# Kernel tuning notes

Measured on AMD Instinct MI355X. Metric: run time of the kernel, lower is better.

The kernel has to match this reference:

```python
import jax, jax.numpy as jnp
import numpy as np

B, S, HID = 1, 2048, 4096
H, HKV = 32, 8
D = HID // H          # 128
G = H // HKV          # 4 query heads per kv head (GQA)


def setup_inputs() -> dict:
    key = jax.random.key(0)
    ks = jax.random.split(key, 5)
    hidden_states = jax.random.normal(ks[0], (B, S, HID), dtype=jnp.float32)
    # additive causal mask: 0 on/below diagonal, large negative above
    causal = jnp.tril(jnp.ones((S, S), dtype=bool))
    attention_mask = jnp.where(causal, 0.0, -1e9).astype(jnp.float32)[None, None]
    sc = 0.02
    wq = jax.random.normal(ks[1], (HID, H * D), dtype=jnp.float32) * sc
    wk = jax.random.normal(ks[2], (HID, HKV * D), dtype=jnp.float32) * sc
    wv = jax.random.normal(ks[3], (HID, HKV * D), dtype=jnp.float32) * sc
    wo = jax.random.normal(ks[4], (H * D, HID), dtype=jnp.float32) * sc
    return {"hidden_states": hidden_states, "attention_mask": attention_mask,
            "wq": wq, "wk": wk, "wv": wv, "wo": wo}


def reference(hidden_states, attention_mask, wq, wk, wv, wo):
    # projections (lora_rank=0 path: plain dense, no bias)
    q = hidden_states @ wq                      # [B,S,H*D]
    k = hidden_states @ wk                      # [B,S,HKV*D]
    v = hidden_states @ wv                      # [B,S,HKV*D]
    # split heads; group query heads by their kv head: head h -> (h//G, h%G)
    q = q.reshape(B, S, HKV, G, D).transpose(0, 2, 3, 1, 4)   # [B,HKV,G,S,D]
    k = k.reshape(B, S, HKV, D).transpose(0, 2, 1, 3)          # [B,HKV,S,D]
    v = v.reshape(B, S, HKV, D).transpose(0, 2, 1, 3)          # [B,HKV,S,D]
    scale = 1.0 / jnp.sqrt(jnp.float32(D))
    # explicit S x S scores (as in source), with GQA kv broadcast over G
    scores = jnp.einsum('bkgsd,bktd->bkgst', q, k) * scale     # [B,HKV,G,S,S]
    scores = scores + attention_mask[:, :, None]               # broadcast over G
    probs = jax.nn.softmax(scores, axis=-1)
    attn = jnp.einsum('bkgst,bktd->bkgsd', probs, v)           # [B,HKV,G,S,D]
    attn = attn.transpose(0, 3, 1, 2, 4).reshape(B, S, H * D)  # [B,S,H*D]
    return attn @ wo                                           # [B,S,HID]
```

## Files before the change

kernel.cpp:

```cpp
#include <hip/hip_runtime.h>
#include <hip/hip_bf16.h>

#define S_LEN 2048
#define HID 4096
#define NH 32
#define NKV 8
#define HD 128
#define LDQKV 6144

typedef __bf16 bf16x8 __attribute__((ext_vector_type(8)));
typedef __bf16 bf16x4 __attribute__((ext_vector_type(4)));
typedef float f32x4 __attribute__((ext_vector_type(4)));

#define GLD16(gp, lp)                                                                   \
    __builtin_amdgcn_global_load_lds((const __attribute__((address_space(1))) void*)(gp), \
                                     (__attribute__((address_space(3))) void*)(lp), 16, 0, 0)

__global__ void cast_bf16_kernel(const float* __restrict__ x, __bf16* __restrict__ y, int n) {
    int i = (blockIdx.x * blockDim.x + threadIdx.x) * 4;
    if (i < n) {
        float4 v = *reinterpret_cast<const float4*>(x + i);
        bf16x4 o;
        o.x = (__bf16)v.x; o.y = (__bf16)v.y; o.z = (__bf16)v.z; o.w = (__bf16)v.w;
        *reinterpret_cast<bf16x4*>(y + i) = o;
    }
}

__global__ void transpose_cast_kernel(const float* __restrict__ W, __bf16* __restrict__ WT,
                                      int K, int N, float scale) {
    __shared__ float tile[32][33];
    int bx = blockIdx.x;
    int by = blockIdx.y;
    int tx = threadIdx.x;
    int ty = threadIdx.y;
    int n = bx * 32 + tx;
#pragma unroll
    for (int i = 0; i < 4; i++) {
        int k = by * 32 + ty + i * 8;
        tile[ty + i * 8][tx] = W[(size_t)k * N + n];
    }
    __syncthreads();
    int k2 = by * 32 + tx;
#pragma unroll
    for (int i = 0; i < 4; i++) {
        int n2 = bx * 32 + ty + i * 8;
        WT[(size_t)n2 * K + k2] = (__bf16)(tile[tx][ty + i * 8] * scale);
    }
}

__global__ void transpose_bf16_kernel(const __bf16* __restrict__ V, int ldin,
                                      __bf16* __restrict__ VT, int ldout) {
    __shared__ __bf16 tile[32][33];
    int bx = blockIdx.x;
    int by = blockIdx.y;
    int tx = threadIdx.x;
    int ty = threadIdx.y;
#pragma unroll
    for (int i = 0; i < 4; i++)
        tile[ty + i * 8][tx] = V[(size_t)(by * 32 + ty + i * 8) * ldin + bx * 32 + tx];
    __syncthreads();
#pragma unroll
    for (int i = 0; i < 4; i++)
        VT[(size_t)(bx * 32 + ty + i * 8) * ldout + by * 32 + tx] = tile[tx][ty + i * 8];
}

template <typename OUT_T>
__global__ __launch_bounds__(256) void gemm_bt_kernel(const __bf16* __restrict__ A, int lda,
                                                      const __bf16* __restrict__ BT, int ldb,
                                                      OUT_T* __restrict__ C, int ldc, int K) {
    __shared__ __bf16 As[128 * 32];
    __shared__ __bf16 Bs[128 * 32];
    int n0 = blockIdx.x * 128;
    int m0 = blockIdx.y * 128;
    int tid = threadIdx.x;
    int wave = tid >> 6, lane = tid & 63, quad = lane >> 4, l16 = lane & 15;
    int wm = (wave >> 1) * 64, wn = (wave & 1) * 64;
    int j0 = wave * 128 + lane;

    f32x4 acc[4][4] = {};

    for (int kb = 0; kb < K; kb += 32) {
        __syncthreads();
#pragma unroll
        for (int q = 0; q < 2; q++) {
            int j = j0 + q * 64;
            int row = j >> 2, col8 = (j & 3) * 8;
            GLD16(&A[(size_t)(m0 + row) * lda + kb + col8], &As[j * 8]);
            GLD16(&BT[(size_t)(n0 + row) * ldb + kb + col8], &Bs[j * 8]);
        }
        __syncthreads();
        bf16x8 af[4], bfr[4];
#pragma unroll
        for (int mt = 0; mt < 4; mt++)
            af[mt] = *reinterpret_cast<const bf16x8*>(&As[(wm + mt * 16 + l16) * 32 + quad * 8]);
#pragma unroll
        for (int nt = 0; nt < 4; nt++)
            bfr[nt] = *reinterpret_cast<const bf16x8*>(&Bs[(wn + nt * 16 + l16) * 32 + quad * 8]);
#pragma unroll
        for (int mt = 0; mt < 4; mt++)
#pragma unroll
            for (int nt = 0; nt < 4; nt++)
                acc[mt][nt] = __builtin_amdgcn_mfma_f32_16x16x32_bf16(af[mt], bfr[nt],
                                                                      acc[mt][nt], 0, 0, 0);
    }

#pragma unroll
    for (int mt = 0; mt < 4; mt++)
#pragma unroll
        for (int nt = 0; nt < 4; nt++)
#pragma unroll
            for (int r = 0; r < 4; r++) {
                int row = m0 + wm + mt * 16 + quad * 4 + r;
                int col = n0 + wn + nt * 16 + l16;
                C[(size_t)row * ldc + col] = (OUT_T)acc[mt][nt][r];
            }
}

__global__ __launch_bounds__(256) void attn_kernel(const __bf16* __restrict__ QKV,
                                                   const __bf16* __restrict__ VT,
                                                   __bf16* __restrict__ Ao,
                                                   __bf16* __restrict__ Opart,
                                                   float* __restrict__ Lp) {
    __shared__ __bf16 Ks[64 * 128];
    __shared__ __bf16 Vs[128 * 64];
    __shared__ __bf16 Pl[4][2][16 * 72];
    int x = blockIdx.x;
    int qt, c;
    if (x < 32) { qt = 31 - (x >> 1); c = x & 1; }
    else        { qt = 47 - x;        c = 0;     }
    int hp = blockIdx.y;
    int kvh = hp >> 1;
    int h0 = kvh * 4 + (hp & 1) * 2;
    int t0 = c ? 16 : 0;
    int t1 = c ? qt : min(qt, 15);
    int tid = threadIdx.x;
    int wave = tid >> 6, lane = tid & 63, quad = lane >> 4, l16 = lane & 15;
    int wq = qt * 64 + wave * 16;
    const __bf16* Kb = QKV + HID + (size_t)kvh * HD;
    const __bf16* Vt = VT + (size_t)kvh * HD * S_LEN;

    bf16x8 qf[2][4];
#pragma unroll
    for (int h = 0; h < 2; h++)
#pragma unroll
        for (int ks = 0; ks < 4; ks++)
            qf[h][ks] = *reinterpret_cast<const bf16x8*>(
                &QKV[(size_t)(wq + l16) * LDQKV + (h0 + h) * HD + ks * 32 + quad * 8]);

    bf16x8 ones;
#pragma unroll
    for (int j = 0; j < 8; j++) ones[j] = (__bf16)1.0f;

    f32x4 acc_o[2][8] = {};
    f32x4 lacc[2] = {};

    for (int t = t0; t <= t1; t++) {
        int kv0 = t << 6;
        bool diag = (t == qt);
        __syncthreads();
#pragma unroll
        for (int i = 0; i < 4; i++) {
            int cc = i * 256 + tid;
            int row = cc >> 4, sub = cc & 15;
            int col8 = sub ^ (row & 15);
            GLD16(&Kb[(size_t)(kv0 + row) * LDQKV + col8 * 8], &Ks[cc * 8]);
        }
#pragma unroll
        for (int i = 0; i < 4; i++) {
            int cc = i * 256 + tid;
            int row = cc >> 3, sub = cc & 7;
            int col8 = sub ^ (row & 7);
            GLD16(&Vt[(size_t)row * S_LEN + kv0 + col8 * 8], &Vs[cc * 8]);
        }
        __syncthreads();

        f32x4 sacc[2][4] = {};
#pragma unroll
        for (int ks = 0; ks < 4; ks++) {
            bf16x8 kf[4];
#pragma unroll
            for (int n = 0; n < 4; n++) {
                int row = n * 16 + l16;
                int sub = (ks * 4 + quad) ^ l16;
                kf[n] = *reinterpret_cast<const bf16x8*>(&Ks[row * 128 + sub * 8]);
            }
#pragma unroll
            for (int n = 0; n < 4; n++) {
                sacc[0][n] = __builtin_amdgcn_mfma_f32_16x16x32_bf16(qf[0][ks], kf[n],
                                                                     sacc[0][n], 0, 0, 0);
                sacc[1][n] = __builtin_amdgcn_mfma_f32_16x16x32_bf16(qf[1][ks], kf[n],
                                                                     sacc[1][n], 0, 0, 0);
            }
        }
#pragma unroll
        for (int h = 0; h < 2; h++) {
            __bf16* Pw = Pl[wave][h];
#pragma unroll
            for (int r = 0; r < 4; r++) {
                int row = wq + quad * 4 + r;
#pragma unroll
                for (int n = 0; n < 4; n++) {
                    float v = sacc[h][n][r];
                    if (diag) {
                        int col = kv0 + n * 16 + l16;
                        if (col > row) v = -1e30f;
                    }
                    Pw[(quad * 4 + r) * 72 + n * 16 + l16] =
                        (__bf16)__builtin_amdgcn_exp2f(v);
                }
            }
        }
#pragma unroll
        for (int ks = 0; ks < 2; ks++) {
            bf16x8 pf0 = *reinterpret_cast<const bf16x8*>(
                &Pl[wave][0][l16 * 72 + ks * 32 + quad * 8]);
            bf16x8 pf1 = *reinterpret_cast<const bf16x8*>(
                &Pl[wave][1][l16 * 72 + ks * 32 + quad * 8]);
            lacc[0] = __builtin_amdgcn_mfma_f32_16x16x32_bf16(pf0, ones, lacc[0], 0, 0, 0);
            lacc[1] = __builtin_amdgcn_mfma_f32_16x16x32_bf16(pf1, ones, lacc[1], 0, 0, 0);
#pragma unroll
            for (int dn = 0; dn < 8; dn++) {
                int row = dn * 16 + l16;
                int sub = (ks * 4 + quad) ^ (row & 7);
                bf16x8 vf = *reinterpret_cast<const bf16x8*>(&Vs[row * 64 + sub * 8]);
                acc_o[0][dn] = __builtin_amdgcn_mfma_f32_16x16x32_bf16(pf0, vf,
                                                                       acc_o[0][dn], 0, 0, 0);
                acc_o[1][dn] = __builtin_amdgcn_mfma_f32_16x16x32_bf16(pf1, vf,
                                                                       acc_o[1][dn], 0, 0, 0);
            }
        }
    }

    if (qt < 16) {
#pragma unroll
        for (int h = 0; h < 2; h++) {
            float rl[4];
#pragma unroll
            for (int r = 0; r < 4; r++) rl[r] = 1.0f / lacc[h][r];
#pragma unroll
            for (int dn = 0; dn < 8; dn++)
#pragma unroll
                for (int r = 0; r < 4; r++) {
                    int row = wq + quad * 4 + r;
                    int col = (h0 + h) * HD + dn * 16 + l16;
                    Ao[(size_t)row * HID + col] = (__bf16)(acc_o[h][dn][r] * rl[r]);
                }
        }
    } else {
        int s = (qt - 16) * 2 + c;
#pragma unroll
        for (int h = 0; h < 2; h++) {
            size_t base = ((size_t)(h0 + h) * 32 + s) * 64 + wave * 16;
#pragma unroll
            for (int dn = 0; dn < 8; dn++)
#pragma unroll
                for (int r = 0; r < 4; r++)
                    Opart[(base + quad * 4 + r) * 128 + dn * 16 + l16] =
                        (__bf16)acc_o[h][dn][r];
            if (l16 == 0) {
#pragma unroll
                for (int r = 0; r < 4; r++)
                    Lp[base + quad * 4 + r] = lacc[h][r];
            }
        }
    }
}

__global__ __launch_bounds__(256) void attn_combine(const __bf16* __restrict__ Opart,
                                                    const float* __restrict__ Lp,
                                                    __bf16* __restrict__ Ao) {
    int qt = 16 + (int)blockIdx.x;
    int h = blockIdx.y;
    int tid = threadIdx.x;
    size_t b0 = ((size_t)h * 32 + (qt - 16) * 2) * 64;
    size_t b1 = b0 + 64;
#pragma unroll 4
    for (int i = 0; i < 32; i++) {
        int el = i * 256 + tid;
        int rl = el >> 7, col = el & 127;
        float l = Lp[b0 + rl] + Lp[b1 + rl];
        float O = (float)Opart[(b0 + rl) * 128 + col] + (float)Opart[(b1 + rl) * 128 + col];
        int row = qt * 64 + rl;
        Ao[(size_t)row * HID + h * HD + col] = (__bf16)(O / l);
    }
}

extern "C" void kernel_launch(void* const* d_in, const int* in_sizes, int n_in,
                              void* d_out, int out_size, void* d_ws, size_t ws_size,
                              hipStream_t stream) {
    const float* hs = (const float*)d_in[0];
    const float* wq = (const float*)d_in[2];
    const float* wk = (const float*)d_in[3];
    const float* wv = (const float*)d_in[4];
    const float* wo = (const float*)d_in[5];
    float* out = (float*)d_out;

    char* ws = (char*)d_ws;
    __bf16* WqkvT = (__bf16*)(ws + (size_t)0);
    __bf16* Opart = (__bf16*)(ws + (size_t)0);
    float*  Lp    = (float*)(ws + ((size_t)20 << 20));
    __bf16* Xb    = (__bf16*)(ws + ((size_t)48 << 20));
    __bf16* QKV   = (__bf16*)(ws + ((size_t)64 << 20));
    __bf16* VTg   = (__bf16*)(ws + ((size_t)88 << 20));
    __bf16* Ab    = Xb;

    const int nX = S_LEN * HID;
    const float SC2 = 0.12751743f;

    cast_bf16_kernel<<<nX / 4 / 256, 256, 0, stream>>>(hs, Xb, nX);
    transpose_cast_kernel<<<dim3(128, 128), dim3(32, 8), 0, stream>>>(wq, WqkvT, HID, HID, SC2);
    transpose_cast_kernel<<<dim3(32, 128), dim3(32, 8), 0, stream>>>(
        wk, WqkvT + (size_t)4096 * HID, HID, NKV * HD, 1.0f);
    transpose_cast_kernel<<<dim3(32, 128), dim3(32, 8), 0, stream>>>(
        wv, WqkvT + (size_t)5120 * HID, HID, NKV * HD, 1.0f);
    gemm_bt_kernel<__bf16><<<dim3(LDQKV / 128, S_LEN / 128), 256, 0, stream>>>(
        Xb, HID, WqkvT, HID, QKV, LDQKV, HID);
    transpose_bf16_kernel<<<dim3(32, 64), dim3(32, 8), 0, stream>>>(
        QKV + 5120, LDQKV, VTg, S_LEN);
    attn_kernel<<<dim3(48, 16), 256, 0, stream>>>(QKV, VTg, Ab, Opart, Lp);
    attn_combine<<<dim3(16, 32), 256, 0, stream>>>(Opart, Lp, Ab);
    transpose_cast_kernel<<<dim3(128, 128), dim3(32, 8), 0, stream>>>(wo, WqkvT, HID, HID, 1.0f);
    gemm_bt_kernel<float><<<dim3(HID / 128, S_LEN / 128), 256, 0, stream>>>(
        Ab, HID, WqkvT, HID, out, HID, HID);
}
```

Baseline: 552.0 us.

## Replace GEMM with 256x256-tile double-buffered swizzled LDS kernel

Replaces the 128x128, single-buffered bf16 GEMM with a 256x256-tile kernel using 512 threads. Each K step stages 64 columns into double-buffered LDS through direct global-to-LDS loads, with an XOR-swizzled layout to avoid bank conflicts. The MFMA work is split into four phases separated by barriers, with wave priority raised around the MFMA bursts. The intent is to overlap the next tile's global loads with compute and to get more reuse per loaded byte. The cost is a much smaller grid (192 and 128 blocks), which may leave many of the GPU's compute units idle, plus about 128KB of LDS per block.

New measurement: 631.0 us. 14.3% more time.

```diff
diff --git a/kernel.cpp b/kernel.cpp
--- a/kernel.cpp
+++ b/kernel.cpp
@@ -64,48 +64,96 @@
         VT[(size_t)(bx * 32 + ty + i * 8) * ldout + by * 32 + tx] = tile[tx][ty + i * 8];
 }
 
+template <int MQ, int NQ>
+__device__ __forceinline__ void gemm_phase(const __bf16* __restrict__ Asb,
+                                           const __bf16* __restrict__ Bsb,
+                                           f32x4 (&acc)[8][4], int wm, int wn,
+                                           int quad, int l16) {
+    bf16x8 af[2][4], bfr[2][2];
+#pragma unroll
+    for (int kk = 0; kk < 2; kk++) {
+        int slot = (kk * 4 + quad) ^ (l16 & 7);
+#pragma unroll
+        for (int i = 0; i < 4; i++) {
+            int row = wm + (MQ * 4 + i) * 16 + l16;
+            af[kk][i] = *reinterpret_cast<const bf16x8*>(&Asb[row * 64 + slot * 8]);
+        }
+#pragma unroll
+        for (int j = 0; j < 2; j++) {
+            int row = wn + (NQ * 2 + j) * 16 + l16;
+            bfr[kk][j] = *reinterpret_cast<const bf16x8*>(&Bsb[row * 64 + slot * 8]);
+        }
+    }
+    __builtin_amdgcn_s_barrier();
+    asm volatile("s_waitcnt lgkmcnt(0)" ::: "memory");
+    __builtin_amdgcn_s_setprio(1);
+#pragma unroll
+    for (int kk = 0; kk < 2; kk++)
+#pragma unroll
+        for (int i = 0; i < 4; i++)
+#pragma unroll
+            for (int j = 0; j < 2; j++)
+                acc[MQ * 4 + i][NQ * 2 + j] = __builtin_amdgcn_mfma_f32_16x16x32_bf16(
+                    af[kk][i], bfr[kk][j], acc[MQ * 4 + i][NQ * 2 + j], 0, 0, 0);
+    __builtin_amdgcn_s_setprio(0);
+    __builtin_amdgcn_s_barrier();
+}
+
 template <typename OUT_T>
-__global__ __launch_bounds__(256) void gemm_bt_kernel(const __bf16* __restrict__ A, int lda,
-                                                      const __bf16* __restrict__ BT, int ldb,
-                                                      OUT_T* __restrict__ C, int ldc, int K) {
-    __shared__ __bf16 As[128 * 32];
-    __shared__ __bf16 Bs[128 * 32];
-    int n0 = blockIdx.x * 128;
-    int m0 = blockIdx.y * 128;
-    int tid = threadIdx.x;
-    int wave = tid >> 6, lane = tid & 63, quad = lane >> 4, l16 = lane & 15;
-    int wm = (wave >> 1) * 64, wn = (wave & 1) * 64;
-    int j0 = wave * 128 + lane;
-
-    f32x4 acc[4][4] = {};
-
-    for (int kb = 0; kb < K; kb += 32) {
-        __syncthreads();
-#pragma unroll
-        for (int q = 0; q < 2; q++) {
-            int j = j0 + q * 64;
-            int row = j >> 2, col8 = (j & 3) * 8;
-            GLD16(&A[(size_t)(m0 + row) * lda + kb + col8], &As[j * 8]);
-            GLD16(&BT[(size_t)(n0 + row) * ldb + kb + col8], &Bs[j * 8]);
-        }
-        __syncthreads();
-        bf16x8 af[4], bfr[4];
-#pragma unroll
-        for (int mt = 0; mt < 4; mt++)
-            af[mt] = *reinterpret_cast<const bf16x8*>(&As[(wm + mt * 16 + l16) * 32 + quad * 8]);
-#pragma unroll
-        for (int nt = 0; nt < 4; nt++)
-            bfr[nt] = *reinterpret_cast<const bf16x8*>(&Bs[(wn + nt * 16 + l16) * 32 + quad * 8]);
-#pragma unroll
-        for (int mt = 0; mt < 4; mt++)
-#pragma unroll
-            for (int nt = 0; nt < 4; nt++)
-                acc[mt][nt] = __builtin_amdgcn_mfma_f32_16x16x32_bf16(af[mt], bfr[nt],
-                                                                      acc[mt][nt], 0, 0, 0);
-    }
-
-#pragma unroll
-    for (int mt = 0; mt < 4; mt++)
+__global__ __launch_bounds__(512, 1) void gemm_bt256_kernel(const __bf16* __restrict__ A, int lda,
+                                                            const __bf16* __restrict__ BT, int ldb,
+                                                            OUT_T* __restrict__ C, int ldc, int K) {
+    __shared__ __bf16 As[2][256 * 64];
+    __shared__ __bf16 Bs[2][256 * 64];
+    const int n0 = blockIdx.x * 256;
+    const int m0 = blockIdx.y * 256;
+    const int tid = threadIdx.x;
+    const int wave = tid >> 6, lane = tid & 63, quad = lane >> 4, l16 = lane & 15;
+    const int wm = (wave >> 2) * 128;
+    const int wn = (wave & 3) * 64;
+
+    f32x4 acc[8][4] = {};
+
+    auto STAGE = [&](int b, int kb) {
+#pragma unroll
+        for (int i = 0; i < 4; i++) {
+            int c = i * 512 + tid;
+            int row = c >> 3;
+            int col8 = (c & 7) ^ (row & 7);
+            GLD16(&A[(size_t)(m0 + row) * lda + kb + col8 * 8], &As[b][c * 8]);
+            GLD16(&BT[(size_t)(n0 + row) * ldb + kb + col8 * 8], &Bs[b][c * 8]);
+        }
+    };
+
+    const int nk = K >> 6;
+    STAGE(0, 0);
+    if (nk > 1) {
+        STAGE(1, 64);
+        asm volatile("s_waitcnt vmcnt(8)" ::: "memory");
+    } else {
+        asm volatile("s_waitcnt vmcnt(0)" ::: "memory");
+    }
+    __builtin_amdgcn_s_barrier();
+
+    for (int kt = 0; kt < nk; ++kt) {
+        const int cur = kt & 1;
+        const __bf16* Asb = As[cur];
+        const __bf16* Bsb = Bs[cur];
+        gemm_phase<0, 0>(Asb, Bsb, acc, wm, wn, quad, l16);
+        gemm_phase<0, 1>(Asb, Bsb, acc, wm, wn, quad, l16);
+        gemm_phase<1, 0>(Asb, Bsb, acc, wm, wn, quad, l16);
+        gemm_phase<1, 1>(Asb, Bsb, acc, wm, wn, quad, l16);
+        if (kt + 2 < nk) {
+            STAGE(cur, (kt + 2) << 6);
+            asm volatile("s_waitcnt vmcnt(8)" ::: "memory");
+        } else {
+            asm volatile("s_waitcnt vmcnt(0)" ::: "memory");
+        }
+        __builtin_amdgcn_s_barrier();
+    }
+
+#pragma unroll
+    for (int mt = 0; mt < 8; mt++)
 #pragma unroll
         for (int nt = 0; nt < 4; nt++)
 #pragma unroll
@@ -313,13 +361,13 @@
         wk, WqkvT + (size_t)4096 * HID, HID, NKV * HD, 1.0f);
     transpose_cast_kernel<<<dim3(32, 128), dim3(32, 8), 0, stream>>>(
         wv, WqkvT + (size_t)5120 * HID, HID, NKV * HD, 1.0f);
-    gemm_bt_kernel<__bf16><<<dim3(LDQKV / 128, S_LEN / 128), 256, 0, stream>>>(
+    gemm_bt256_kernel<__bf16><<<dim3(LDQKV / 256, S_LEN / 256), 512, 0, stream>>>(
         Xb, HID, WqkvT, HID, QKV, LDQKV, HID);
     transpose_bf16_kernel<<<dim3(32, 64), dim3(32, 8), 0, stream>>>(
         QKV + 5120, LDQKV, VTg, S_LEN);
     attn_kernel<<<dim3(48, 16), 256, 0, stream>>>(QKV, VTg, Ab, Opart, Lp);
     attn_combine<<<dim3(16, 32), 256, 0, stream>>>(Opart, Lp, Ab);
     transpose_cast_kernel<<<dim3(128, 128), dim3(32, 8), 0, stream>>>(wo, WqkvT, HID, HID, 1.0f);
-    gemm_bt_kernel<float><<<dim3(HID / 128, S_LEN / 128), 256, 0, stream>>>(
+    gemm_bt256_kernel<float><<<dim3(HID / 256, S_LEN / 256), 512, 0, stream>>>(
         Ab, HID, WqkvT, HID, out, HID, HID);
 }
```

## Add 256x256 double-buffered pipelined GEMM for the QKV projection

Applied to the files above, without the earlier changes.

Adds a new 512-thread GEMM kernel with 256x256 tiles, BK=64 double-buffered LDS staging, XOR swizzle, and an interleaved schedule. Global-to-LDS prefetches for k-tile kt+2 are issued between quarter MFMA phases, and s_setprio is raised around the MFMA blocks. Only the QKV projection uses it, to get more data reuse per tile and overlap loads with compute. The grid is now 24x8 = 192 blocks, which may underfill the GPU's CUs. The output projection still uses the old kernel.

Result: faster. 537.4 us (-2.6%).

```diff
diff --git a/kernel.cpp b/kernel.cpp
--- a/kernel.cpp
+++ b/kernel.cpp
@@ -15,6 +15,8 @@
 #define GLD16(gp, lp)                                                                   \
     __builtin_amdgcn_global_load_lds((const __attribute__((address_space(1))) void*)(gp), \
                                      (__attribute__((address_space(3))) void*)(lp), 16, 0, 0)
+
+#define MFMA_BF16(a, b, c) __builtin_amdgcn_mfma_f32_16x16x32_bf16((a), (b), (c), 0, 0, 0)
 
 __global__ void cast_bf16_kernel(const float* __restrict__ x, __bf16* __restrict__ y, int n) {
     int i = (blockIdx.x * blockDim.x + threadIdx.x) * 4;
@@ -100,8 +102,7 @@
         for (int mt = 0; mt < 4; mt++)
 #pragma unroll
             for (int nt = 0; nt < 4; nt++)
-                acc[mt][nt] = __builtin_amdgcn_mfma_f32_16x16x32_bf16(af[mt], bfr[nt],
-                                                                      acc[mt][nt], 0, 0, 0);
+                acc[mt][nt] = MFMA_BF16(af[mt], bfr[nt], acc[mt][nt]);
     }
 
 #pragma unroll
@@ -113,6 +114,153 @@
                 int row = m0 + wm + mt * 16 + quad * 4 + r;
                 int col = n0 + wn + nt * 16 + l16;
                 C[(size_t)row * ldc + col] = (OUT_T)acc[mt][nt][r];
+            }
+}
+
+template <typename OUT_T>
+__global__ __launch_bounds__(512, 1) void gemm_bt256_kernel(const __bf16* __restrict__ A, int lda,
+                                                            const __bf16* __restrict__ BT, int ldb,
+                                                            OUT_T* __restrict__ C, int ldc, int K) {
+    __shared__ __bf16 As[2][256 * 64];
+    __shared__ __bf16 Bs[2][256 * 64];
+    const int n0 = blockIdx.x * 256;
+    const int m0 = blockIdx.y * 256;
+    const int tid = threadIdx.x;
+    const int lane = tid & 63, quad = lane >> 4, l16 = lane & 15;
+    const int wave = tid >> 6;
+    const int wg64 = (wave >> 2) * 64;
+    const int wn32 = (wave & 3) * 32;
+
+    f32x4 acc[8][4] = {};
+
+    auto STAGE_A = [&](int b, int kb, int round) {
+        int c = round * 512 + tid;
+        int row = c >> 3;
+        int col8 = (c & 7) ^ (row & 7);
+        GLD16(&A[(size_t)(m0 + row) * lda + kb + col8 * 8], &As[b][c * 8]);
+    };
+    auto STAGE_B = [&](int b, int kb, int round) {
+        int c = round * 512 + tid;
+        int row = c >> 3;
+        int col8 = (c & 7) ^ (row & 7);
+        GLD16(&BT[(size_t)(n0 + row) * ldb + kb + col8 * 8], &Bs[b][c * 8]);
+    };
+
+    const int nk = K >> 6;
+#pragma unroll
+    for (int r = 0; r < 4; r++) { STAGE_A(0, 0, r); STAGE_B(0, 0, r); }
+#pragma unroll
+    for (int r = 0; r < 4; r++) { STAGE_A(1, 64, r); STAGE_B(1, 64, r); }
+    asm volatile("s_waitcnt vmcnt(8)" ::: "memory");
+    __builtin_amdgcn_s_barrier();
+
+    for (int kt = 0; kt < nk; ++kt) {
+        const int cur = kt & 1;
+        const __bf16* Asb = As[cur];
+        const __bf16* Bsb = Bs[cur];
+        const int kb2 = (kt + 2) << 6;
+        const bool pf = (kt + 2) < nk;
+
+        bf16x8 af[2][4], blo[2][2], bhi[2][2];
+
+#pragma unroll
+        for (int kk = 0; kk < 2; kk++) {
+            int slot = ((kk * 4 + quad) ^ (l16 & 7)) * 8;
+#pragma unroll
+            for (int i = 0; i < 4; i++)
+                af[kk][i] = *reinterpret_cast<const bf16x8*>(
+                    &Asb[(wg64 + i * 16 + l16) * 64 + slot]);
+#pragma unroll
+            for (int j = 0; j < 2; j++)
+                blo[kk][j] = *reinterpret_cast<const bf16x8*>(
+                    &Bsb[(wn32 + j * 16 + l16) * 64 + slot]);
+        }
+        __builtin_amdgcn_s_barrier();
+        asm volatile("s_waitcnt lgkmcnt(0)" ::: "memory");
+        __builtin_amdgcn_s_setprio(1);
+#pragma unroll
+        for (int kk = 0; kk < 2; kk++)
+#pragma unroll
+            for (int i = 0; i < 4; i++)
+#pragma unroll
+                for (int j = 0; j < 2; j++)
+                    acc[i][j] = MFMA_BF16(af[kk][i], blo[kk][j], acc[i][j]);
+        __builtin_amdgcn_s_setprio(0);
+        __builtin_amdgcn_s_barrier();
+
+#pragma unroll
+        for (int kk = 0; kk < 2; kk++) {
+            int slot = ((kk * 4 + quad) ^ (l16 & 7)) * 8;
+#pragma unroll
+            for (int j = 0; j < 2; j++)
+                bhi[kk][j] = *reinterpret_cast<const bf16x8*>(
+                    &Bsb[(wn32 + 128 + j * 16 + l16) * 64 + slot]);
+        }
+        if (pf) { STAGE_A(cur, kb2, 0); STAGE_A(cur, kb2, 1); }
+        __builtin_amdgcn_s_barrier();
+        asm volatile("s_waitcnt lgkmcnt(0)" ::: "memory");
+        __builtin_amdgcn_s_setprio(1);
+#pragma unroll
+        for (int kk = 0; kk < 2; kk++)
+#pragma unroll
+            for (int i = 0; i < 4; i++)
+#pragma unroll
+                for (int j = 0; j < 2; j++)
+                    acc[i][j + 2] = MFMA_BF16(af[kk][i], bhi[kk][j], acc[i][j + 2]);
+        __builtin_amdgcn_s_setprio(0);
+        __builtin_amdgcn_s_barrier();
+
+#pragma unroll
+        for (int kk = 0; kk < 2; kk++) {
+            int slot = ((kk * 4 + quad) ^ (l16 & 7)) * 8;
+#pragma unroll
+            for (int i = 0; i < 4; i++)
+                af[kk][i] = *reinterpret_cast<const bf16x8*>(
+                    &Asb[(wg64 + 128 + i * 16 + l16) * 64 + slot]);
+        }
+        if (pf) { STAGE_B(cur, kb2, 0); STAGE_B(cur, kb2, 1); }
+        __builtin_amdgcn_s_barrier();
+        asm volatile("s_waitcnt lgkmcnt(0)" ::: "memory");
+        __builtin_amdgcn_s_setprio(1);
+#pragma unroll
+        for (int kk = 0; kk < 2; kk++)
+#pragma unroll
+            for (int i = 0; i < 4; i++)
+#pragma unroll
+                for (int j = 0; j < 2; j++)
+                    acc[i + 4][j + 2] = MFMA_BF16(af[kk][i], bhi[kk][j], acc[i + 4][j + 2]);
+        __builtin_amdgcn_s_setprio(0);
+        __builtin_amdgcn_s_barrier();
+
+        if (pf) { STAGE_A(cur, kb2, 2); STAGE_A(cur, kb2, 3);
+                  STAGE_B(cur, kb2, 2); STAGE_B(cur, kb2, 3); }
+        __builtin_amdgcn_s_barrier();
+        __builtin_amdgcn_s_setprio(1);
+#pragma unroll
+        for (int kk = 0; kk < 2; kk++)
+#pragma unroll
+            for (int i = 0; i < 4; i++)
+#pragma unroll
+                for (int j = 0; j < 2; j++)
+                    acc[i + 4][j] = MFMA_BF16(af[kk][i], blo[kk][j], acc[i + 4][j]);
+        __builtin_amdgcn_s_setprio(0);
+        if (pf) {
+            asm volatile("s_waitcnt vmcnt(8)" ::: "memory");
+        } else {
+            asm volatile("s_waitcnt vmcnt(0)" ::: "memory");
+        }
+        __builtin_amdgcn_s_barrier();
+    }
+
+#pragma unroll
+    for (int i = 0; i < 8; i++)
+#pragma unroll
+        for (int j = 0; j < 4; j++)
+#pragma unroll
+            for (int r = 0; r < 4; r++) {
+                int row = m0 + wg64 + (i & 3) * 16 + (i >> 2) * 128 + quad * 4 + r;
+                int col = n0 + wn32 + (j & 1) * 16 + (j >> 1) * 128 + l16;
+                C[(size_t)row * ldc + col] = (OUT_T)acc[i][j][r];
             }
 }
 
@@ -186,10 +334,8 @@
             }
 #pragma unroll
             for (int n = 0; n < 4; n++) {
-                sacc[0][n] = __builtin_amdgcn_mfma_f32_16x16x32_bf16(qf[0][ks], kf[n],
-                                                                     sacc[0][n], 0, 0, 0);
-                sacc[1][n] = __builtin_amdgcn_mfma_f32_16x16x32_bf16(qf[1][ks], kf[n],
-                                                                     sacc[1][n], 0, 0, 0);
+                sacc[0][n] = MFMA_BF16(qf[0][ks], kf[n], sacc[0][n]);
+                sacc[1][n] = MFMA_BF16(qf[1][ks], kf[n], sacc[1][n]);
             }
         }
 #pragma unroll
@@ -216,17 +362,15 @@
                 &Pl[wave][0][l16 * 72 + ks * 32 + quad * 8]);
             bf16x8 pf1 = *reinterpret_cast<const bf16x8*>(
                 &Pl[wave][1][l16 * 72 + ks * 32 + quad * 8]);
-            lacc[0] = __builtin_amdgcn_mfma_f32_16x16x32_bf16(pf0, ones, lacc[0], 0, 0, 0);
-            lacc[1] = __builtin_amdgcn_mfma_f32_16x16x32_bf16(pf1, ones, lacc[1], 0, 0, 0);
+            lacc[0] = MFMA_BF16(pf0, ones, lacc[0]);
+            lacc[1] = MFMA_BF16(pf1, ones, lacc[1]);
 #pragma unroll
             for (int dn = 0; dn < 8; dn++) {
                 int row = dn * 16 + l16;
                 int sub = (ks * 4 + quad) ^ (row & 7);
                 bf16x8 vf = *reinterpret_cast<const bf16x8*>(&Vs[row * 64 + sub * 8]);
-                acc_o[0][dn] = __builtin_amdgcn_mfma_f32_16x16x32_bf16(pf0, vf,
-                                                                       acc_o[0][dn], 0, 0, 0);
-                acc_o[1][dn] = __builtin_amdgcn_mfma_f32_16x16x32_bf16(pf1, vf,
-                                                                       acc_o[1][dn], 0, 0, 0);
+                acc_o[0][dn] = MFMA_BF16(pf0, vf, acc_o[0][dn]);
+                acc_o[1][dn] = MFMA_BF16(pf1, vf, acc_o[1][dn]);
             }
         }
     }
@@ -313,7 +457,7 @@
         wk, WqkvT + (size_t)4096 * HID, HID, NKV * HD, 1.0f);
     transpose_cast_kernel<<<dim3(32, 128), dim3(32, 8), 0, stream>>>(
         wv, WqkvT + (size_t)5120 * HID, HID, NKV * HD, 1.0f);
-    gemm_bt_kernel<__bf16><<<dim3(LDQKV / 128, S_LEN / 128), 256, 0, stream>>>(
+    gemm_bt256_kernel<__bf16><<<dim3(LDQKV / 256, S_LEN / 256), 512, 0, stream>>>(
         Xb, HID, WqkvT, HID, QKV, LDQKV, HID);
     transpose_bf16_kernel<<<dim3(32, 64), dim3(32, 8), 0, stream>>>(
         QKV + 5120, LDQKV, VTg, S_LEN);
```
